# Kernel tuning notes

Hardware: AMD Instinct MI355X
Metric: run time of the kernel (lower is better)

## Reference

```python
import jax, jax.numpy as jnp
import numpy as np

Q_MAX = 127.0  # symmetric int8 range

def setup_inputs() -> dict:
    key = jax.random.key(0)
    k1, k2, k3, k4 = jax.random.split(key, 4)
    B, S, K, N = 4, 2048, 4096, 4096
    inp = jax.random.normal(k1, (B, S, K), dtype=jnp.float32)
    # int8 weight in [-127, 127], stored via randint(0,255)-127 per spec
    qweight = (jax.random.randint(k2, (N, K), 0, 255) - 127).astype(jnp.int8)
    # per-out-channel weight dequant scales (small positive)
    wparams = (jax.random.uniform(k3, (N,), dtype=jnp.float32) * 0.02 + 0.001)
    bias = jax.random.normal(k4, (N,), dtype=jnp.float32) * 0.1
    return {"inp": inp, "qweight": qweight, "wparams": wparams, "bias": bias}

def reference(inp, qweight, wparams, bias):
    # inp: [B, S, K] float32; qweight: [N, K] int8; wparams: [N]; bias: [N]
    B, S, K = inp.shape
    x = inp.reshape(B * S, K)
    # qntz: per-row symmetric absmax quantization of the activation to int8
    a_scale = jnp.max(jnp.abs(x), axis=1, keepdims=True) / Q_MAX  # [M, 1]
    qinp = jnp.clip(jnp.round(x / a_scale), -Q_MAX, Q_MAX).astype(jnp.int8)  # [M, K]
    d = jax.lax.dot_general(qinp, qweight.T, (((1,), (0,)), ((), ())),
                            preferred_element_type=jnp.int32)  # [M, N]
    # dqntz: scale by per-row act scale and per-col weight scale, add bias
    out = d.astype(jnp.float32) * a_scale * wparams[None, :] + bias[None, :]
    return out.reshape(B, S, -1)
```

## Files before the change

### kernel.cpp

```cpp
#include <hip/hip_runtime.h>
#include <hip/hip_bf16.h>


using int32x4 = __attribute__((ext_vector_type(4))) int;

#define QMAXF 127.0f

__global__ __launch_bounds__(256) void repack_weights(
    const int* __restrict__ w, signed char* __restrict__ w8, int total)
{
    bool is32 = true;
#pragma unroll
    for (int i = 0; i < 16; ++i) {
        int v = w[i];
        is32 = is32 && (v >= -127 && v <= 127);
    }

    const int t = blockIdx.x * blockDim.x + threadIdx.x;
    const int nth = gridDim.x * blockDim.x;
    const int chunks = total / 16;

    if (is32) {
        for (int c = t; c < chunks; c += nth) {
            const int32x4* src = reinterpret_cast<const int32x4*>(w + (size_t)c * 16);
            int32x4 a0 = src[0], a1 = src[1], a2 = src[2], a3 = src[3];
            int32x4 o;
            o[0] = (a0[0] & 0xff) | ((a0[1] & 0xff) << 8) | ((a0[2] & 0xff) << 16) | ((a0[3] & 0xff) << 24);
            o[1] = (a1[0] & 0xff) | ((a1[1] & 0xff) << 8) | ((a1[2] & 0xff) << 16) | ((a1[3] & 0xff) << 24);
            o[2] = (a2[0] & 0xff) | ((a2[1] & 0xff) << 8) | ((a2[2] & 0xff) << 16) | ((a2[3] & 0xff) << 24);
            o[3] = (a3[0] & 0xff) | ((a3[1] & 0xff) << 8) | ((a3[2] & 0xff) << 16) | ((a3[3] & 0xff) << 24);
            reinterpret_cast<int32x4*>(w8)[c] = o;
        }
    } else {
        const int32x4* src = reinterpret_cast<const int32x4*>(w);
        int32x4* dst = reinterpret_cast<int32x4*>(w8);
        for (int c = t; c < chunks; c += nth) dst[c] = src[c];
    }
}

__global__ __launch_bounds__(256) void quant_rows(
    const float* __restrict__ x, signed char* __restrict__ q,
    float* __restrict__ scale, int K)
{
    const int row = blockIdx.x;
    const int t = threadIdx.x;
    const float4* xr = reinterpret_cast<const float4*>(x + (size_t)row * K);

    float4 v[4];
    float m = 0.f;
#pragma unroll
    for (int i = 0; i < 4; ++i) {
        v[i] = xr[t + i * 256];
        m = fmaxf(m, fmaxf(fmaxf(fabsf(v[i].x), fabsf(v[i].y)),
                           fmaxf(fabsf(v[i].z), fabsf(v[i].w))));
    }
#pragma unroll
    for (int off = 32; off >= 1; off >>= 1)
        m = fmaxf(m, __shfl_xor(m, off, 64));
    __shared__ float wmax[4];
    const int wave = t >> 6;
    if ((t & 63) == 0) wmax[wave] = m;
    __syncthreads();
    m = fmaxf(fmaxf(wmax[0], wmax[1]), fmaxf(wmax[2], wmax[3]));

    const float s   = m / QMAXF;
    const float inv = (m > 0.f) ? (QMAXF / m) : 0.f;
    if (t == 0) scale[row] = s;

    int* qr = reinterpret_cast<int*>(q + (size_t)row * K);
#pragma unroll
    for (int i = 0; i < 4; ++i) {
        const float* f = reinterpret_cast<const float*>(&v[i]);
        unsigned int packed = 0;
#pragma unroll
        for (int j = 0; j < 4; ++j) {
            int qi = __float2int_rn(f[j] * inv);
            qi = qi > 127 ? 127 : (qi < -127 ? -127 : qi);
            packed |= ((unsigned int)(qi & 0xff)) << (8 * j);
        }
        qr[t + i * 256] = (int)packed;
    }
}

#define BM 256
#define BN 256
#define BKB 64
#define NBUF 4

__device__ __forceinline__ void async_copy16(const void* g, void* lds) {
    __builtin_amdgcn_global_load_lds(
        (const __attribute__((address_space(1))) void*)g,
        (__attribute__((address_space(3))) void*)lds, 16, 0, 0);
}

#define BARF do {                                         \
    __builtin_amdgcn_sched_barrier(0);                    \
    asm volatile("" ::: "memory");                        \
    __builtin_amdgcn_s_barrier();                         \
    asm volatile("" ::: "memory");                        \
    __builtin_amdgcn_sched_barrier(0);                    \
} while (0)

#define LGKM0 asm volatile("s_waitcnt lgkmcnt(0)" ::: "memory")
#define VM4   asm volatile("s_waitcnt vmcnt(4)" ::: "memory")
#define VM0   asm volatile("s_waitcnt vmcnt(0)" ::: "memory")

__global__ __launch_bounds__(512, 2) void gemm_i8_dequant_ov(
    const signed char* __restrict__ A,
    const signed char* __restrict__ B,
    const float* __restrict__ a_scale,
    const float* __restrict__ wparams,
    const float* __restrict__ bias,
    float* __restrict__ out,
    int M, int N, int K)
{
    __shared__ __align__(16) signed char lds[NBUF * 32768];

    const int t    = threadIdx.x;
    const int lane = t & 63;
    const int wave = t >> 6;
    const int wr   = wave >> 2;
    const int wc   = wave & 3;

    const int nwg = gridDim.x;
    const int cpx = nwg >> 3;
    const int swz = (blockIdx.x & 7) * cpx + (blockIdx.x >> 3);
    const int nbx = N / BN;
    const int rowBase = (swz / nbx) * BM;
    const int colBase = (swz % nbx) * BN;

    const int r15 = lane & 15;
    const int ksl = lane >> 4;

    int32x4 acc[8][4] = {};
    const int NT = K / BKB;

    const signed char* gA0 = A + (size_t)(rowBase + wave * 16 + r15)       * K + ksl * 16;
    const signed char* gA1 = A + (size_t)(rowBase + (8 + wave) * 16 + r15) * K + ksl * 16;
    const signed char* gB0 = B + (size_t)(colBase + wave * 16 + r15)       * K + ksl * 16;
    const signed char* gB1 = B + (size_t)(colBase + (8 + wave) * 16 + r15) * K + ksl * 16;

    auto stage = [&](int tile) {
        signed char* L = lds + (tile & (NBUF - 1)) * 32768;
        const size_t kt = (size_t)tile * BKB;
        async_copy16(gA0 + kt, L + wave * 1024);
        async_copy16(gA1 + kt, L + (8 + wave) * 1024);
        async_copy16(gB0 + kt, L + 16384 + wave * 1024);
        async_copy16(gB1 + kt, L + 16384 + (8 + wave) * 1024);
    };
    auto ldFrags = [&](int tile, int32x4 (&fa)[8], int32x4 (&fb)[4]) {
        const signed char* Ab = lds + (tile & (NBUF - 1)) * 32768 + wr * 8192 + lane * 16;
        const signed char* Bb = lds + (tile & (NBUF - 1)) * 32768 + 16384 + wc * 4096 + lane * 16;
#pragma unroll
        for (int mm = 0; mm < 8; ++mm)
            fa[mm] = *reinterpret_cast<const int32x4*>(Ab + mm * 1024);
#pragma unroll
        for (int nn = 0; nn < 4; ++nn)
            fb[nn] = *reinterpret_cast<const int32x4*>(Bb + nn * 1024);
    };
    auto mfmaAll = [&](const int32x4 (&fa)[8], const int32x4 (&fb)[4]) {
        __builtin_amdgcn_s_setprio(1);
#pragma unroll
        for (int mm = 0; mm < 8; ++mm)
#pragma unroll
            for (int nn = 0; nn < 4; ++nn)
                acc[mm][nn] = __builtin_amdgcn_mfma_i32_16x16x64_i8(
                    fa[mm], fb[nn], acc[mm][nn], 0, 0, 0);
        __builtin_amdgcn_s_setprio(0);
    };

    int32x4 cA[8], cB[4], nA[8], nB[4];

    stage(0); stage(1); stage(2);
    VM4;
    BARF;
    ldFrags(0, cA, cB);

    for (int tt = 0; tt + 1 < NT - 3; tt += 2) {
        stage(tt + 3);
        ldFrags(tt + 1, nA, nB);
        mfmaAll(cA, cB);
        VM4; LGKM0; BARF;

        stage(tt + 4);
        ldFrags(tt + 2, cA, cB);
        mfmaAll(nA, nB);
        VM4; LGKM0; BARF;
    }

    stage(NT - 1);
    ldFrags(NT - 3, nA, nB);
    mfmaAll(cA, cB);
    VM4; LGKM0; BARF;

    ldFrags(NT - 2, cA, cB);
    mfmaAll(nA, nB);
    VM0; LGKM0; BARF;

    ldFrags(NT - 1, nA, nB);
    mfmaAll(cA, cB);

    mfmaAll(nA, nB);

#pragma unroll
    for (int mm = 0; mm < 8; ++mm) {
        const int rb = rowBase + wr * 128 + mm * 16 + ksl * 4;
        float asc[4];
#pragma unroll
        for (int r = 0; r < 4; ++r) asc[r] = a_scale[rb + r];
#pragma unroll
        for (int nn = 0; nn < 4; ++nn) {
            const int col = colBase + wc * 64 + nn * 16 + r15;
            const float wp = wparams[col];
            const float bs = bias[col];
#pragma unroll
            for (int r = 0; r < 4; ++r) {
                out[(size_t)(rb + r) * N + col] =
                    (float)acc[mm][nn][r] * asc[r] * wp + bs;
            }
        }
    }
}

extern "C" void kernel_launch(void* const* d_in, const int* in_sizes, int n_in,
                              void* d_out, int out_size, void* d_ws, size_t ws_size,
                              hipStream_t stream) {
    const float* inp     = (const float*)d_in[0];
    const int*   qw_raw  = (const int*)d_in[1];
    const float* wparams = (const float*)d_in[2];
    const float* bias    = (const float*)d_in[3];
    float*       out     = (float*)d_out;

    const int N = in_sizes[2];
    const int K = in_sizes[1] / N;
    const int M = in_sizes[0] / K;

    signed char* qinp    = (signed char*)d_ws;
    float*       a_scale = (float*)((char*)d_ws + (size_t)M * K);
    size_t off_w8 = (size_t)M * K + (((size_t)M * sizeof(float) + 255) & ~(size_t)255);
    signed char* w8      = (signed char*)((char*)d_ws + off_w8);

    repack_weights<<<2048, 256, 0, stream>>>(qw_raw, w8, N * K);
    quant_rows<<<M, 256, 0, stream>>>(inp, qinp, a_scale, K);

    const int nwg = (M / BM) * (N / BN);
    gemm_i8_dequant_ov<<<nwg, 512, 0, stream>>>(
        qinp, w8, a_scale, wparams, bias, out, M, N, K);
}
```

Before: 203.5 us.

## Switch GEMM to 32x32x32 int8 MFMA with matching LDS fragment layout

Replaces the 16x16x64 int8 MFMA tiling with 32x32x32 int8 MFMA instructions. Global-to-LDS staging and fragment loads are remapped so each 32-row fragment holds two 32-byte K slices, and the epilogue is rewritten for the 32x32 accumulator layout. Each wave issues fewer, larger MFMAs per tile, which raises the arithmetic done per LDS fragment read. In exchange the accumulator layout changes and the dequantized output stores follow a different row pattern.

```diff
diff --git a/kernel.cpp b/kernel.cpp
--- a/kernel.cpp
+++ b/kernel.cpp
@@ -2,7 +2,8 @@
 #include <hip/hip_bf16.h>
 
 
-using int32x4 = __attribute__((ext_vector_type(4))) int;
+using int32x4  = __attribute__((ext_vector_type(4)))  int;
+using int32x16 = __attribute__((ext_vector_type(16))) int;
 
 #define QMAXF 127.0f
 
@@ -105,7 +106,7 @@
 #define VM4   asm volatile("s_waitcnt vmcnt(4)" ::: "memory")
 #define VM0   asm volatile("s_waitcnt vmcnt(0)" ::: "memory")
 
-__global__ __launch_bounds__(512, 2) void gemm_i8_dequant_ov(
+__global__ __launch_bounds__(512, 2) void gemm_i8_dequant_32(
     const signed char* __restrict__ A,
     const signed char* __restrict__ B,
     const float* __restrict__ a_scale,
@@ -129,47 +130,63 @@
     const int rowBase = (swz / nbx) * BM;
     const int colBase = (swz % nbx) * BN;
 
-    const int r15 = lane & 15;
-    const int ksl = lane >> 4;
-
-    int32x4 acc[8][4] = {};
+    const int l31 = lane & 31;
+    const int hi  = lane >> 5;
+
+    int32x16 acc[4][2] = {};
     const int NT = K / BKB;
 
-    const signed char* gA0 = A + (size_t)(rowBase + wave * 16 + r15)       * K + ksl * 16;
-    const signed char* gA1 = A + (size_t)(rowBase + (8 + wave) * 16 + r15) * K + ksl * 16;
-    const signed char* gB0 = B + (size_t)(colBase + wave * 16 + r15)       * K + ksl * 16;
-    const signed char* gB1 = B + (size_t)(colBase + (8 + wave) * 16 + r15) * K + ksl * 16;
+    const int fid0 = wave, fid1 = 8 + wave;
+    const signed char* gA0 = A + (size_t)(rowBase + (fid0 >> 1) * 32 + l31) * K
+                               + (fid0 & 1) * 32 + hi * 16;
+    const signed char* gA1 = A + (size_t)(rowBase + (fid1 >> 1) * 32 + l31) * K
+                               + (fid1 & 1) * 32 + hi * 16;
+    const signed char* gB0 = B + (size_t)(colBase + (fid0 >> 1) * 32 + l31) * K
+                               + (fid0 & 1) * 32 + hi * 16;
+    const signed char* gB1 = B + (size_t)(colBase + (fid1 >> 1) * 32 + l31) * K
+                               + (fid1 & 1) * 32 + hi * 16;
 
     auto stage = [&](int tile) {
         signed char* L = lds + (tile & (NBUF - 1)) * 32768;
         const size_t kt = (size_t)tile * BKB;
-        async_copy16(gA0 + kt, L + wave * 1024);
-        async_copy16(gA1 + kt, L + (8 + wave) * 1024);
-        async_copy16(gB0 + kt, L + 16384 + wave * 1024);
-        async_copy16(gB1 + kt, L + 16384 + (8 + wave) * 1024);
+        async_copy16(gA0 + kt, L + fid0 * 1024);
+        async_copy16(gA1 + kt, L + fid1 * 1024);
+        async_copy16(gB0 + kt, L + 16384 + fid0 * 1024);
+        async_copy16(gB1 + kt, L + 16384 + fid1 * 1024);
     };
-    auto ldFrags = [&](int tile, int32x4 (&fa)[8], int32x4 (&fb)[4]) {
-        const signed char* Ab = lds + (tile & (NBUF - 1)) * 32768 + wr * 8192 + lane * 16;
-        const signed char* Bb = lds + (tile & (NBUF - 1)) * 32768 + 16384 + wc * 4096 + lane * 16;
-#pragma unroll
-        for (int mm = 0; mm < 8; ++mm)
-            fa[mm] = *reinterpret_cast<const int32x4*>(Ab + mm * 1024);
-#pragma unroll
-        for (int nn = 0; nn < 4; ++nn)
-            fb[nn] = *reinterpret_cast<const int32x4*>(Bb + nn * 1024);
+
+    auto ldFrags = [&](int tile, int32x4 (&fa)[4][2], int32x4 (&fb)[2][2]) {
+        const signed char* base = lds + (tile & (NBUF - 1)) * 32768;
+        const signed char* Ab = base + (wr * 4) * 2048 + lane * 16;
+        const signed char* Bb = base + 16384 + (wc * 2) * 2048 + lane * 16;
+#pragma unroll
+        for (int mm = 0; mm < 4; ++mm)
+#pragma unroll
+            for (int sl = 0; sl < 2; ++sl)
+                fa[mm][sl] = *reinterpret_cast<const int32x4*>(
+                    Ab + (mm * 2 + sl) * 1024);
+#pragma unroll
+        for (int nn = 0; nn < 2; ++nn)
+#pragma unroll
+            for (int sl = 0; sl < 2; ++sl)
+                fb[nn][sl] = *reinterpret_cast<const int32x4*>(
+                    Bb + (nn * 2 + sl) * 1024);
     };
-    auto mfmaAll = [&](const int32x4 (&fa)[8], const int32x4 (&fb)[4]) {
+
+    auto mfmaAll = [&](const int32x4 (&fa)[4][2], const int32x4 (&fb)[2][2]) {
         __builtin_amdgcn_s_setprio(1);
 #pragma unroll
-        for (int mm = 0; mm < 8; ++mm)
-#pragma unroll
-            for (int nn = 0; nn < 4; ++nn)
-                acc[mm][nn] = __builtin_amdgcn_mfma_i32_16x16x64_i8(
-                    fa[mm], fb[nn], acc[mm][nn], 0, 0, 0);
+        for (int sl = 0; sl < 2; ++sl)
+#pragma unroll
+            for (int mm = 0; mm < 4; ++mm)
+#pragma unroll
+                for (int nn = 0; nn < 2; ++nn)
+                    acc[mm][nn] = __builtin_amdgcn_mfma_i32_32x32x32_i8(
+                        fa[mm][sl], fb[nn][sl], acc[mm][nn], 0, 0, 0);
         __builtin_amdgcn_s_setprio(0);
     };
 
-    int32x4 cA[8], cB[4], nA[8], nB[4];
+    int32x4 cA[4][2], cB[2][2], nA[4][2], nB[2][2];
 
     stage(0); stage(1); stage(2);
     VM4;
@@ -199,24 +216,26 @@
 
     ldFrags(NT - 1, nA, nB);
     mfmaAll(cA, cB);
-
     mfmaAll(nA, nB);
 
 #pragma unroll
-    for (int mm = 0; mm < 8; ++mm) {
-        const int rb = rowBase + wr * 128 + mm * 16 + ksl * 4;
-        float asc[4];
-#pragma unroll
-        for (int r = 0; r < 4; ++r) asc[r] = a_scale[rb + r];
-#pragma unroll
-        for (int nn = 0; nn < 4; ++nn) {
-            const int col = colBase + wc * 64 + nn * 16 + r15;
+    for (int mm = 0; mm < 4; ++mm) {
+        const int rb = rowBase + wr * 128 + mm * 32;
+        float asc[16];
+#pragma unroll
+        for (int q = 0; q < 4; ++q)
+            *reinterpret_cast<float4*>(&asc[q * 4]) =
+                *reinterpret_cast<const float4*>(&a_scale[rb + 8 * q + 4 * hi]);
+#pragma unroll
+        for (int nn = 0; nn < 2; ++nn) {
+            const int col = colBase + wc * 64 + nn * 32 + l31;
             const float wp = wparams[col];
             const float bs = bias[col];
 #pragma unroll
-            for (int r = 0; r < 4; ++r) {
-                out[(size_t)(rb + r) * N + col] =
-                    (float)acc[mm][nn][r] * asc[r] * wp + bs;
+            for (int reg = 0; reg < 16; ++reg) {
+                const int row = rb + (reg & 3) + 8 * (reg >> 2) + 4 * hi;
+                out[(size_t)row * N + col] =
+                    (float)acc[mm][nn][reg] * asc[reg] * wp + bs;
             }
         }
     }
@@ -244,6 +263,6 @@
     quant_rows<<<M, 256, 0, stream>>>(inp, qinp, a_scale, K);
 
     const int nwg = (M / BM) * (N / BN);
-    gemm_i8_dequant_ov<<<nwg, 512, 0, stream>>>(
+    gemm_i8_dequant_32<<<nwg, 512, 0, stream>>>(
         qinp, w8, a_scale, wparams, bias, out, M, N, K);
 }
```

Result: slower. 216.7 us (+6.5%).
